# Performance work log

Measured on AMD Instinct MI355X. Metric: run time of the kernel, lower is better.

The kernel has to match this reference:

```python
import jax, jax.numpy as jnp
import numpy as np

B, C, S, H = 64, 64, 128, 512   # batch, num_centroid, max_seq_length, hidden_size
D = S * H
EPS = 1e-8


def setup_inputs() -> dict:
    key = jax.random.key(0)
    k1, k2 = jax.random.split(key)
    return {
        "input": jax.random.normal(k1, (B, D), dtype=jnp.float32),
        "centroid_weight": jax.random.normal(k2, (C, D), dtype=jnp.float32),
    }


def _gram(x):
    # x: (..., S, H) -> (..., S, S)
    return jnp.einsum('...sh,...th->...st', x, x)


def _centering(g):
    # H @ g @ H with H = I - 11^T/n  ==  g - rowmean - colmean + grandmean
    rm = jnp.mean(g, axis=-1, keepdims=True)
    cm = jnp.mean(g, axis=-2, keepdims=True)
    gm = jnp.mean(g, axis=(-1, -2), keepdims=True)
    return g - rm - cm + gm


def reference(input, centroid_weight):
    # torch.cdist(input, centroid_weight), p=2
    x2 = jnp.sum(input * input, axis=1, keepdims=True)        # (B,1)
    w2 = jnp.sum(centroid_weight * centroid_weight, axis=1)   # (C,)
    d2 = x2 + w2[None, :] - 2.0 * (input @ centroid_weight.T)
    dist = jnp.sqrt(jnp.maximum(d2, 0.0))                     # (B,C)

    xb = input.reshape(B, S, H)
    cw = centroid_weight.reshape(C, S, H)

    cgx = _centering(_gram(xb))   # (B,S,S)
    cgy = _centering(_gram(cw))   # (C,S,S)

    # linear HSIC(x,y) summed over last two dims, broadcast (B,1)x(C) -> (B,C)
    hxy = jnp.einsum('bst,cst->bc', cgx, cgy)
    hxx = jnp.sum(cgx * cgx, axis=(-1, -2))   # (B,)
    hyy = jnp.sum(cgy * cgy, axis=(-1, -2))   # (C,)
    cka_mat = -jnp.log(
        jnp.abs(hxy / (jnp.sqrt(hxx)[:, None] * jnp.sqrt(hyy)[None, :])) + EPS
    )  # (B,C)

    idx = jnp.argmax(cka_mat, axis=-1)                 # (B,)
    sel = centroid_weight[idx].reshape(B, S, H)        # selected centroids
    cgs = _centering(_gram(sel))                       # (B,S,S)

    # second CKA: x is (B,1,S,S), y is (B,S,S) -> broadcast to (B,B) as in torch
    hxy2 = jnp.einsum('bst,cst->bc', cgx, cgs)         # (B,B)
    hyy2 = jnp.sum(cgs * cgs, axis=(-1, -2))           # (B,)
    ratio = jnp.abs(hxy2 / (jnp.sqrt(hxx)[:, None] * jnp.sqrt(hyy2)[None, :]))
    cka_loss = -jnp.log(jnp.mean(ratio) + EPS)         # scalar

    return (cka_loss, dist, centroid_weight, idx)
```

## Files before the change

kernel.cpp:

```cpp
#include <hip/hip_runtime.h>
#include <math.h>

#define Bn 64
#define Cn 64
#define Sn 128
#define Hn 512
#define Dn 65536
#define SSn 16384

using f32x4 = __attribute__((ext_vector_type(4))) float;
using bf16x8 = __attribute__((ext_vector_type(8))) short;

__device__ __forceinline__ float wredf(float v) {
#pragma unroll
    for (int o = 32; o > 0; o >>= 1) v += __shfl_down(v, o, 64);
    return v;
}

__device__ __forceinline__ unsigned short f2bf(float f) {
    unsigned int u = __float_as_uint(f);
    u += 0x7fffu + ((u >> 16) & 1u);
    return (unsigned short)(u >> 16);
}
__device__ __forceinline__ float bf2f(unsigned short h) {
    return __uint_as_float(((unsigned int)h) << 16);
}

__global__ __launch_bounds__(512) void kA(const float* __restrict__ x,
                                          const float* __restrict__ w,
                                          float* __restrict__ gF,
                                          float* __restrict__ rsT,
                                          float* __restrict__ hpartG,
                                          float* __restrict__ x2,
                                          float* __restrict__ w2,
                                          float* __restrict__ partials,
                                          float* __restrict__ outcpy) {
    __shared__ __align__(16) unsigned char smem[67584];
    const int bid = blockIdx.x;
    const int tid = threadIdx.x;
    const int lane = tid & 63;
    const int wv = tid >> 6;
    const int lrow = lane & 15;
    const int lk8 = (lane >> 4) * 8;
    const int crow4 = (lane >> 4) * 4;
    if (bid < 128) {
        __shared__ float sA[8], sB[8];
        const int mat = bid;
        const int wm = wv >> 1;
        const int wc = wv & 1;
        const float* src = (mat < Bn) ? (x + (size_t)mat * Dn) : (w + (size_t)(mat - Bn) * Dn);
        unsigned short (*hi)[72] = (unsigned short(*)[72])smem;
        unsigned short (*lo)[72] = (unsigned short(*)[72])(smem + 18432);
        f32x4 acc[2][4] = {};
        float ssq = 0.f;
        float4 cur[4], nxt[4];
#pragma unroll
        for (int p = 0; p < 4; ++p) {
            const int f = tid + 512 * p;
            cur[p] = *(const float4*)(src + (size_t)(f >> 4) * Hn + (f & 15) * 4);
        }
        for (int c = 0; c < 8; ++c) {
#pragma unroll
            for (int p = 0; p < 4; ++p) {
                const int f = tid + 512 * p;
                const int r = f >> 4, c4 = (f & 15) * 4;
                float4 v = cur[p];
                ssq += v.x * v.x + v.y * v.y + v.z * v.z + v.w * v.w;
                unsigned short h0 = f2bf(v.x), h1 = f2bf(v.y), h2 = f2bf(v.z), h3 = f2bf(v.w);
                *(ushort4*)&hi[r][c4] = make_ushort4(h0, h1, h2, h3);
                *(ushort4*)&lo[r][c4] = make_ushort4(f2bf(v.x - bf2f(h0)), f2bf(v.y - bf2f(h1)),
                                                     f2bf(v.z - bf2f(h2)), f2bf(v.w - bf2f(h3)));
            }
            if (c < 7) {
#pragma unroll
                for (int p = 0; p < 4; ++p) {
                    const int f = tid + 512 * p;
                    nxt[p] = *(const float4*)(src + (size_t)(f >> 4) * Hn + (c + 1) * 64 + (f & 15) * 4);
                }
            }
            __syncthreads();
#pragma unroll
            for (int ks = 0; ks < 64; ks += 32) {
                bf16x8 ah[2], al[2];
#pragma unroll
                for (int i = 0; i < 2; ++i) {
                    const int arow = wm * 32 + i * 16 + lrow;
                    ah[i] = *(const bf16x8*)&hi[arow][ks + lk8];
                    al[i] = *(const bf16x8*)&lo[arow][ks + lk8];
                }
#pragma unroll
                for (int j = 0; j < 4; ++j) {
                    const int brow = wc * 64 + j * 16 + lrow;
                    bf16x8 bh = *(const bf16x8*)&hi[brow][ks + lk8];
                    bf16x8 bl = *(const bf16x8*)&lo[brow][ks + lk8];
#pragma unroll
                    for (int i = 0; i < 2; ++i) {
                        acc[i][j] = __builtin_amdgcn_mfma_f32_16x16x32_bf16(ah[i], bh, acc[i][j], 0, 0, 0);
                        acc[i][j] = __builtin_amdgcn_mfma_f32_16x16x32_bf16(ah[i], bl, acc[i][j], 0, 0, 0);
                        acc[i][j] = __builtin_amdgcn_mfma_f32_16x16x32_bf16(al[i], bh, acc[i][j], 0, 0, 0);
                    }
                }
            }
            __syncthreads();
            if (c < 7) {
#pragma unroll
                for (int p = 0; p < 4; ++p) cur[p] = nxt[p];
            }
        }
        float* dst = gF + (size_t)mat * SSn + wv * 2048;
        float sq = 0.f;
#pragma unroll
        for (int i = 0; i < 2; ++i)
#pragma unroll
            for (int j = 0; j < 4; ++j) {
                f32x4 v = acc[i][j];
                sq += v[0] * v[0] + v[1] * v[1] + v[2] * v[2] + v[3] * v[3];
                *(f32x4*)(dst + (i * 4 + j) * 256 + lane * 4) = v;
            }
        float* sRS = (float*)smem;
#pragma unroll
        for (int i = 0; i < 2; ++i)
#pragma unroll
            for (int r = 0; r < 4; ++r) {
                float rs = acc[i][0][r] + acc[i][1][r] + acc[i][2][r] + acc[i][3][r];
                rs += __shfl_xor(rs, 1, 64);
                rs += __shfl_xor(rs, 2, 64);
                rs += __shfl_xor(rs, 4, 64);
                rs += __shfl_xor(rs, 8, 64);
                if (lrow == 0) sRS[(wm * 32 + i * 16 + crow4 + r) * 2 + wc] = rs;
            }
        sq = wredf(sq);
        ssq = wredf(ssq);
        if (lane == 0) { sA[wv] = sq; sB[wv] = ssq; }
        __syncthreads();
        if (tid < 128) rsT[(size_t)tid * 128 + mat] = sRS[tid * 2] + sRS[tid * 2 + 1];
        if (tid == 0) {
            float g2 = 0.f, tr = 0.f;
#pragma unroll
            for (int i = 0; i < 8; ++i) { g2 += sA[i]; tr += sB[i]; }
            hpartG[mat] = g2;
            if (mat < Bn) x2[mat] = tr; else w2[mat - Bn] = tr;
        }
    } else {
        const int did = bid - 128;
        unsigned short (*la)[264] = (unsigned short(*)[264])smem;
        unsigned short (*lb)[264] = (unsigned short(*)[264])(smem + 33792);
        const int rg = wv >> 1, cgb = (wv & 1) * 2;
        f32x4 acc[2] = {};
        for (int cc = 0; cc < 2; ++cc) {
            const int k0 = did * 512 + cc * 256;
            __syncthreads();
#pragma unroll
            for (int p = 0; p < 8; ++p) {
                const int f = tid + 512 * p;
                const int row = f >> 6, c4 = (f & 63) * 4;
                float4 vx = *(const float4*)(x + (size_t)row * Dn + k0 + c4);
                float4 vw = *(const float4*)(w + (size_t)row * Dn + k0 + c4);
                *(ushort4*)&la[row][c4] = make_ushort4(f2bf(vx.x), f2bf(vx.y), f2bf(vx.z), f2bf(vx.w));
                *(ushort4*)&lb[row][c4] = make_ushort4(f2bf(vw.x), f2bf(vw.y), f2bf(vw.z), f2bf(vw.w));
                float* dc = outcpy + (size_t)row * Dn + k0 + c4;
                dc[0] = vw.x; dc[1] = vw.y; dc[2] = vw.z; dc[3] = vw.w;
            }
            __syncthreads();
#pragma unroll
            for (int ks = 0; ks < 8; ++ks) {
                bf16x8 a = *(const bf16x8*)&la[rg * 16 + lrow][ks * 32 + lk8];
#pragma unroll
                for (int q = 0; q < 2; ++q) {
                    bf16x8 b = *(const bf16x8*)&lb[(cgb + q) * 16 + lrow][ks * 32 + lk8];
                    acc[q] = __builtin_amdgcn_mfma_f32_16x16x32_bf16(a, b, acc[q], 0, 0, 0);
                }
            }
        }
        float* p = partials + (size_t)did * 4096;
#pragma unroll
        for (int q = 0; q < 2; ++q)
#pragma unroll
            for (int r = 0; r < 4; ++r)
                p[(rg * 16 + crow4 + r) * 64 + (cgb + q) * 16 + lrow] = acc[q][r];
    }
}

__global__ __launch_bounds__(256) void kB(const float* __restrict__ gF,
                                          const float* __restrict__ partials,
                                          const float* __restrict__ rsT,
                                          const float* __restrict__ hpartG,
                                          const float* __restrict__ x2,
                                          const float* __restrict__ w2,
                                          float* __restrict__ partials2,
                                          float* __restrict__ Sv,
                                          float* __restrict__ hxx,
                                          float* __restrict__ hyy,
                                          float* __restrict__ od) {
    __shared__ __align__(16) unsigned char smem[65536];
    const int bid = blockIdx.x;
    const int tid = threadIdx.x;
    if (bid < 64) {
        float (*la)[68] = (float(*)[68])smem;
        float (*lb)[68] = (float(*)[68])(smem + 17408);
        const int slc = (tid & 15) * 4;
        const int ry = tid >> 4, tx = tid & 15;
        float acc[4][4] = {};
        for (int c = 0; c < 4; ++c) {
            const int k0 = bid * 256 + c * 64;
            __syncthreads();
            for (int r = tid >> 4; r < 64; r += 16) {
                *(float4*)&la[r][slc] = *(const float4*)(gF + (size_t)r * SSn + k0 + slc);
                *(float4*)&lb[r][slc] = *(const float4*)(gF + (size_t)(64 + r) * SSn + k0 + slc);
            }
            __syncthreads();
            for (int k = 0; k < 64; k += 4) {
                float4 av[4], bv[4];
#pragma unroll
                for (int i = 0; i < 4; ++i) av[i] = *(const float4*)&la[4 * ry + i][k];
#pragma unroll
                for (int j = 0; j < 4; ++j) bv[j] = *(const float4*)&lb[16 * j + tx][k];
#pragma unroll
                for (int i = 0; i < 4; ++i)
#pragma unroll
                    for (int j = 0; j < 4; ++j)
                        acc[i][j] += av[i].x * bv[j].x + av[i].y * bv[j].y +
                                     av[i].z * bv[j].z + av[i].w * bv[j].w;
            }
        }
        float* p = partials2 + (size_t)bid * 4096;
#pragma unroll
        for (int i = 0; i < 4; ++i)
#pragma unroll
            for (int j = 0; j < 4; ++j)
                p[(4 * ry + i) * 64 + 16 * j + tx] = acc[i][j];
    } else if (bid < 128) {
        double* red = (double*)smem;
        const int b2 = bid - 64;
        const int o = tid & 63, sl = tid >> 6;
        const int i = b2 * 64 + o;
        double s = 0;
        for (int t = 0; t < 32; ++t)
            s += (double)partials[(size_t)(sl + 4 * t) * 4096 + i];
        red[sl * 64 + o] = s;
        __syncthreads();
        if (tid < 64) {
            double t = red[tid] + red[64 + tid] + red[128 + tid] + red[192 + tid];
            float d2 = x2[b2] + w2[tid] - 2.f * (float)t;
            od[b2 * 64 + tid] = sqrtf(fmaxf(d2, 0.f));
        }
    } else {
        float* rl = (float*)smem;
        for (int p = 0; p < 16; ++p) {
            const int f4 = tid + 256 * p;
            *(float4*)(rl + 4 * f4) = *(const float4*)(rsT + 4 * f4);
        }
        __syncthreads();
        if (tid < 128) {
            float s = 0.f, q = 0.f;
            for (int t = 0; t < 128; ++t) {
                float v = rl[t * 128 + tid];
                s += v; q += v * v;
            }
            Sv[tid] = s;
            double val = (double)hpartG[tid] - (double)q * (1.0 / 64.0)
                       + (double)s * (double)s * (1.0 / 16384.0);
            if (tid < 64) hxx[tid] = (float)val; else hyy[tid - 64] = (float)val;
        }
    }
}

__global__ __launch_bounds__(256) void kC(const float* __restrict__ partials2,
                                          const float* __restrict__ rsT,
                                          const float* __restrict__ Sv,
                                          double* __restrict__ hxy) {
    __shared__ double red[256];
    const int b = blockIdx.x;
    const int o = threadIdx.x & 63;
    const int sl = threadIdx.x >> 6;
    const int i = b * 64 + o;
    double s = 0;
    for (int t = 0; t < 16; ++t)
        s += (double)partials2[(size_t)(sl + 4 * t) * 4096 + i];
    double corr = 0;
    for (int t = 0; t < 32; ++t) {
        const int ss = sl * 32 + t;
        corr += (double)rsT[ss * 128 + b] * (double)rsT[ss * 128 + 64 + o];
    }
    red[sl * 64 + o] = s - corr * (1.0 / 64.0);
    __syncthreads();
    if (threadIdx.x < 64) {
        double t = red[threadIdx.x] + red[64 + threadIdx.x] +
                   red[128 + threadIdx.x] + red[192 + threadIdx.x];
        t += (double)Sv[b] * (double)Sv[64 + threadIdx.x] * (1.0 / 16384.0);
        hxy[b * 64 + threadIdx.x] = t;
    }
}

__global__ void finalize_k(const double* __restrict__ hxy, const float* __restrict__ hxx,
                           const float* __restrict__ hyy, float* __restrict__ out0,
                           float* __restrict__ oidx) {
    __shared__ double inv_sx[64], inv_sy[64];
    __shared__ double qv[256];
    __shared__ int qi[256];
    __shared__ int sidx[64];
    __shared__ double sred[4];
    const int tid = threadIdx.x;
    if (tid < 64) {
        inv_sx[tid] = 1.0 / sqrt((double)hxx[tid]);
        inv_sy[tid] = 1.0 / sqrt((double)hyy[tid]);
    }
    __syncthreads();
    {
        const int b = tid >> 2, q = tid & 3;
        double best = 1e300; int bi = 64;
        for (int c = q * 16; c < q * 16 + 16; ++c) {
            double v = fabs(hxy[b * 64 + c]) * inv_sy[c];
            if (v < best) { best = v; bi = c; }
        }
        qv[tid] = best; qi[tid] = bi;
    }
    __syncthreads();
    if (tid < 64) {
        double best = qv[4 * tid]; int bi = qi[4 * tid];
        for (int q = 1; q < 4; ++q) {
            if (qv[4 * tid + q] < best) { best = qv[4 * tid + q]; bi = qi[4 * tid + q]; }
        }
        sidx[tid] = bi;
        oidx[tid] = (float)bi;
    }
    __syncthreads();
    double s = 0.0;
    for (int e = tid; e < 4096; e += 256) {
        const int b = e >> 6, c = e & 63;
        const int ic = sidx[c];
        s += fabs(hxy[b * 64 + ic]) * inv_sx[b] * inv_sy[ic];
    }
#pragma unroll
    for (int o = 32; o > 0; o >>= 1) s += __shfl_down(s, o, 64);
    if ((tid & 63) == 0) sred[tid >> 6] = s;
    __syncthreads();
    if (tid == 0) {
        double t = sred[0] + sred[1] + sred[2] + sred[3];
        out0[0] = (float)(-log(t / 4096.0 + 1e-8));
    }
}

extern "C" void kernel_launch(void* const* d_in, const int* in_sizes, int n_in,
                              void* d_out, int out_size, void* d_ws, size_t ws_size,
                              hipStream_t stream) {
    const float* x = (const float*)d_in[0];
    const float* w = (const float*)d_in[1];
    float* out = (float*)d_out;
    float* ws = (float*)d_ws;
    float* gF        = ws;
    float* partials  = ws + 2097152;
    float* partials2 = ws + 2621440;
    float* rsT       = ws + 2883584;
    float* hpartG    = ws + 2899968;
    float* Sv        = ws + 2900096;
    float* x2        = ws + 2900224;
    float* w2        = ws + 2900288;
    float* hxx       = ws + 2900352;
    float* hyy       = ws + 2900416;
    double* hxyD     = (double*)(ws + 2900480);

    kA<<<256, 512, 0, stream>>>(x, w, gF, rsT, hpartG, x2, w2, partials, out + 4097);
    kB<<<129, 256, 0, stream>>>(gF, partials, rsT, hpartG, x2, w2,
                                partials2, Sv, hxx, hyy, out + 1);
    kC<<<64, 256, 0, stream>>>(partials2, rsT, Sv, hxyD);
    finalize_k<<<1, 256, 0, stream>>>(hxyD, hxx, hyy, out, out + 4198401);
}
```

Measured before the change: 117.3 us.

## Shrink LDS footprints, use hip bf16 intrinsics, and accumulate hxy partials in double

The distance blocks in kA now stage 128-column chunks in four passes instead of 256-column chunks in two, which cuts kA's shared memory roughly in half and may allow more resident blocks per CU. The bf16 hi/lo split now uses the HIP bfloat16 intrinsics. kB accumulates each chunk's cross-Gram products in double and writes double partials, which doubles that buffer's traffic but reduces float rounding error in hxy. The row-sum reduction in kB reads rsT directly from global memory instead of staging it in LDS, so kB's LDS allocation also shrinks.

```diff
diff --git a/kernel.cpp b/kernel.cpp
--- a/kernel.cpp
+++ b/kernel.cpp
@@ -1,4 +1,5 @@
 #include <hip/hip_runtime.h>
+#include <hip/hip_bf16.h>
 #include <math.h>
 
 #define Bn 64
@@ -18,12 +19,17 @@
 }
 
 __device__ __forceinline__ unsigned short f2bf(float f) {
-    unsigned int u = __float_as_uint(f);
-    u += 0x7fffu + ((u >> 16) & 1u);
-    return (unsigned short)(u >> 16);
-}
-__device__ __forceinline__ float bf2f(unsigned short h) {
-    return __uint_as_float(((unsigned int)h) << 16);
+    __hip_bfloat16 h = __float2bfloat16(f);
+    unsigned short u;
+    __builtin_memcpy(&u, &h, 2);
+    return u;
+}
+__device__ __forceinline__ void split2(float f, unsigned short& hi, unsigned short& lo) {
+    __hip_bfloat16 h = __float2bfloat16(f);
+    float rem = f - __bfloat162float(h);
+    __hip_bfloat16 l = __float2bfloat16(rem);
+    __builtin_memcpy(&hi, &h, 2);
+    __builtin_memcpy(&lo, &l, 2);
 }
 
 __global__ __launch_bounds__(512) void kA(const float* __restrict__ x,
@@ -35,7 +41,7 @@
                                           float* __restrict__ w2,
                                           float* __restrict__ partials,
                                           float* __restrict__ outcpy) {
-    __shared__ __align__(16) unsigned char smem[67584];
+    __shared__ __align__(16) unsigned char smem[36864];
     const int bid = blockIdx.x;
     const int tid = threadIdx.x;
     const int lane = tid & 63;
@@ -66,10 +72,11 @@
                 const int r = f >> 4, c4 = (f & 15) * 4;
                 float4 v = cur[p];
                 ssq += v.x * v.x + v.y * v.y + v.z * v.z + v.w * v.w;
-                unsigned short h0 = f2bf(v.x), h1 = f2bf(v.y), h2 = f2bf(v.z), h3 = f2bf(v.w);
-                *(ushort4*)&hi[r][c4] = make_ushort4(h0, h1, h2, h3);
-                *(ushort4*)&lo[r][c4] = make_ushort4(f2bf(v.x - bf2f(h0)), f2bf(v.y - bf2f(h1)),
-                                                     f2bf(v.z - bf2f(h2)), f2bf(v.w - bf2f(h3)));
+                ushort4 vh, vl;
+                split2(v.x, vh.x, vl.x); split2(v.y, vh.y, vl.y);
+                split2(v.z, vh.z, vl.z); split2(v.w, vh.w, vl.w);
+                *(ushort4*)&hi[r][c4] = vh;
+                *(ushort4*)&lo[r][c4] = vl;
             }
             if (c < 7) {
 #pragma unroll
@@ -143,17 +150,17 @@
         }
     } else {
         const int did = bid - 128;
-        unsigned short (*la)[264] = (unsigned short(*)[264])smem;
-        unsigned short (*lb)[264] = (unsigned short(*)[264])(smem + 33792);
+        unsigned short (*la)[136] = (unsigned short(*)[136])smem;
+        unsigned short (*lb)[136] = (unsigned short(*)[136])(smem + 17408);
         const int rg = wv >> 1, cgb = (wv & 1) * 2;
         f32x4 acc[2] = {};
-        for (int cc = 0; cc < 2; ++cc) {
-            const int k0 = did * 512 + cc * 256;
-            __syncthreads();
-#pragma unroll
-            for (int p = 0; p < 8; ++p) {
+        for (int cc = 0; cc < 4; ++cc) {
+            const int k0 = did * 512 + cc * 128;
+            __syncthreads();
+#pragma unroll
+            for (int p = 0; p < 4; ++p) {
                 const int f = tid + 512 * p;
-                const int row = f >> 6, c4 = (f & 63) * 4;
+                const int row = f >> 5, c4 = (f & 31) * 4;
                 float4 vx = *(const float4*)(x + (size_t)row * Dn + k0 + c4);
                 float4 vw = *(const float4*)(w + (size_t)row * Dn + k0 + c4);
                 *(ushort4*)&la[row][c4] = make_ushort4(f2bf(vx.x), f2bf(vx.y), f2bf(vx.z), f2bf(vx.w));
@@ -163,7 +170,7 @@
             }
             __syncthreads();
 #pragma unroll
-            for (int ks = 0; ks < 8; ++ks) {
+            for (int ks = 0; ks < 4; ++ks) {
                 bf16x8 a = *(const bf16x8*)&la[rg * 16 + lrow][ks * 32 + lk8];
 #pragma unroll
                 for (int q = 0; q < 2; ++q) {
@@ -187,12 +194,12 @@
                                           const float* __restrict__ hpartG,
                                           const float* __restrict__ x2,
                                           const float* __restrict__ w2,
-                                          float* __restrict__ partials2,
+                                          double* __restrict__ partials2,
                                           float* __restrict__ Sv,
                                           float* __restrict__ hxx,
                                           float* __restrict__ hyy,
                                           float* __restrict__ od) {
-    __shared__ __align__(16) unsigned char smem[65536];
+    __shared__ __align__(16) unsigned char smem[34816];
     const int bid = blockIdx.x;
     const int tid = threadIdx.x;
     if (bid < 64) {
@@ -200,7 +207,7 @@
         float (*lb)[68] = (float(*)[68])(smem + 17408);
         const int slc = (tid & 15) * 4;
         const int ry = tid >> 4, tx = tid & 15;
-        float acc[4][4] = {};
+        double accd[4][4] = {};
         for (int c = 0; c < 4; ++c) {
             const int k0 = bid * 256 + c * 64;
             __syncthreads();
@@ -209,6 +216,7 @@
                 *(float4*)&lb[r][slc] = *(const float4*)(gF + (size_t)(64 + r) * SSn + k0 + slc);
             }
             __syncthreads();
+            float acc[4][4] = {};
             for (int k = 0; k < 64; k += 4) {
                 float4 av[4], bv[4];
 #pragma unroll
@@ -222,13 +230,17 @@
                         acc[i][j] += av[i].x * bv[j].x + av[i].y * bv[j].y +
                                      av[i].z * bv[j].z + av[i].w * bv[j].w;
             }
-        }
-        float* p = partials2 + (size_t)bid * 4096;
+#pragma unroll
+            for (int i = 0; i < 4; ++i)
+#pragma unroll
+                for (int j = 0; j < 4; ++j) accd[i][j] += (double)acc[i][j];
+        }
+        double* p = partials2 + (size_t)bid * 4096;
 #pragma unroll
         for (int i = 0; i < 4; ++i)
 #pragma unroll
             for (int j = 0; j < 4; ++j)
-                p[(4 * ry + i) * 64 + 16 * j + tx] = acc[i][j];
+                p[(4 * ry + i) * 64 + 16 * j + tx] = accd[i][j];
     } else if (bid < 128) {
         double* red = (double*)smem;
         const int b2 = bid - 64;
@@ -245,16 +257,11 @@
             od[b2 * 64 + tid] = sqrtf(fmaxf(d2, 0.f));
         }
     } else {
-        float* rl = (float*)smem;
-        for (int p = 0; p < 16; ++p) {
-            const int f4 = tid + 256 * p;
-            *(float4*)(rl + 4 * f4) = *(const float4*)(rsT + 4 * f4);
-        }
-        __syncthreads();
         if (tid < 128) {
             float s = 0.f, q = 0.f;
+#pragma unroll 4
             for (int t = 0; t < 128; ++t) {
-                float v = rl[t * 128 + tid];
+                float v = rsT[t * 128 + tid];
                 s += v; q += v * v;
             }
             Sv[tid] = s;
@@ -265,7 +272,7 @@
     }
 }
 
-__global__ __launch_bounds__(256) void kC(const float* __restrict__ partials2,
+__global__ __launch_bounds__(256) void kC(const double* __restrict__ partials2,
                                           const float* __restrict__ rsT,
                                           const float* __restrict__ Sv,
                                           double* __restrict__ hxy) {
@@ -276,7 +283,7 @@
     const int i = b * 64 + o;
     double s = 0;
     for (int t = 0; t < 16; ++t)
-        s += (double)partials2[(size_t)(sl + 4 * t) * 4096 + i];
+        s += partials2[(size_t)(sl + 4 * t) * 4096 + i];
     double corr = 0;
     for (int t = 0; t < 32; ++t) {
         const int ss = sl * 32 + t;
@@ -350,15 +357,15 @@
     float* ws = (float*)d_ws;
     float* gF        = ws;
     float* partials  = ws + 2097152;
-    float* partials2 = ws + 2621440;
-    float* rsT       = ws + 2883584;
-    float* hpartG    = ws + 2899968;
-    float* Sv        = ws + 2900096;
-    float* x2        = ws + 2900224;
-    float* w2        = ws + 2900288;
-    float* hxx       = ws + 2900352;
-    float* hyy       = ws + 2900416;
-    double* hxyD     = (double*)(ws + 2900480);
+    double* partials2 = (double*)(ws + 2621440);
+    float* rsT       = ws + 3670016;
+    float* hpartG    = ws + 3686400;
+    float* Sv        = ws + 3686528;
+    float* x2        = ws + 3686656;
+    float* w2        = ws + 3686720;
+    float* hxx       = ws + 3686784;
+    float* hyy       = ws + 3686848;
+    double* hxyD     = (double*)(ws + 3686912);
 
     kA<<<256, 512, 0, stream>>>(x, w, gF, rsT, hpartG, x2, w2, partials, out + 4097);
     kB<<<129, 256, 0, stream>>>(gF, partials, rsT, hpartG, x2, w2,
```

Result: no change. 116.9 us (-0.3%).
